# Optimization experiments

Hardware: AMD Instinct MI355X
Metric: run time of the kernel (lower is better)

Reference implementation:

```python
import jax, jax.numpy as jnp
import numpy as np

DIM = 1024
HEADS = 16
HEAD_DIM = DIM // HEADS
MLP_HID = 4 * DIM
EPS = 1e-5


def layer_norm(x, g, b):
    mu = jnp.mean(x, axis=-1, keepdims=True)
    var = jnp.mean(jnp.square(x - mu), axis=-1, keepdims=True)
    return (x - mu) * jax.lax.rsqrt(var + EPS) * g + b


def setup_inputs() -> dict:
    key = jax.random.key(0)
    ks = jax.random.split(key, 8)
    s_in = 1.0 / np.sqrt(DIM)
    s_hid = 1.0 / np.sqrt(MLP_HID)
    return {
        "x": jax.random.normal(ks[0], (4, 2048, DIM), dtype=jnp.float32),
        "qkv_w": jax.random.uniform(ks[1], (3 * DIM, DIM), jnp.float32, -s_in, s_in),
        "proj_w": jax.random.uniform(ks[2], (DIM, DIM), jnp.float32, -s_in, s_in),
        "proj_b": jnp.zeros((DIM,), jnp.float32),
        "ln1_g": jnp.ones((DIM,), jnp.float32),
        "ln1_b": jnp.zeros((DIM,), jnp.float32),
        "w1": jax.random.uniform(ks[3], (MLP_HID, DIM), jnp.float32, -s_in, s_in),
        "b1": jnp.zeros((MLP_HID,), jnp.float32),
        "prelu_a": jnp.asarray(0.25, jnp.float32),
        "w2": jax.random.uniform(ks[4], (DIM, MLP_HID), jnp.float32, -s_hid, s_hid),
        "b2": jnp.zeros((DIM,), jnp.float32),
        "ln2_g": jnp.ones((DIM,), jnp.float32),
        "ln2_b": jnp.zeros((DIM,), jnp.float32),
    }


def reference(x, qkv_w, proj_w, proj_b, ln1_g, ln1_b, w1, b1, prelu_a, w2, b2, ln2_g, ln2_b):
    B, N, C = x.shape
    scale = HEAD_DIM ** (-0.5)

    # Multi-head self-attention (full NxN scores, softmax over keys)
    qkv = (x @ qkv_w.T).reshape(B, N, 3, HEADS, HEAD_DIM)
    qkv = jnp.transpose(qkv, (2, 0, 3, 1, 4))  # [3, B, H, N, hd]
    q, k, v = qkv[0] * scale, qkv[1], qkv[2]
    attn = jax.nn.softmax(jnp.einsum("bhnd,bhmd->bhnm", q, k), axis=-1)
    o = jnp.einsum("bhnm,bhmd->bhnd", attn, v)
    o = jnp.transpose(o, (0, 2, 1, 3)).reshape(B, N, C)
    o = o @ proj_w.T + proj_b

    # Post-norm residual 1
    x = layer_norm(x + o, ln1_g, ln1_b)

    # MLP: Linear -> (Dropout=identity in eval) -> PReLU -> Linear
    h = x @ w1.T + b1
    h = jnp.where(h >= 0, h, prelu_a * h)
    h = h @ w2.T + b2

    # Post-norm residual 2
    return layer_norm(x + h, ln2_g, ln2_b)
```

## Files before the change

### kernel.cpp

```cpp
#include <hip/hip_runtime.h>


typedef __attribute__((ext_vector_type(8))) short short8;
typedef __attribute__((ext_vector_type(4))) short short4v;
typedef __attribute__((ext_vector_type(4))) float floatx4;
typedef __attribute__((ext_vector_type(4))) int int4v;

__device__ __forceinline__ float bf2f(unsigned short u) {
    return __uint_as_float(((unsigned int)u) << 16);
}
__device__ __forceinline__ unsigned short f2bf(float f) {
    unsigned int u = __float_as_uint(f);
    u += 0x7FFFu + ((u >> 16) & 1u);
    return (unsigned short)(u >> 16);
}
__device__ __forceinline__ int pack2bf(float a, float b) {
    return (int)f2bf(a) | ((int)f2bf(b) << 16);
}
__device__ __forceinline__ unsigned int cvt_pk_bf16(float lo, float hi) {
    unsigned int r;
    asm("v_cvt_pk_bf16_f32 %0, %1, %2" : "=v"(r) : "v"(lo), "v"(hi));
    return r;
}

#define Q_PRESCALE 0.18033688011112043f

#if __has_builtin(__builtin_amdgcn_exp2f)
__device__ __forceinline__ float fast_exp2(float x) { return __builtin_amdgcn_exp2f(x); }
#else
__device__ __forceinline__ float fast_exp2(float x) { return __expf(x * 0.6931471805599453f); }
#endif

#if __has_builtin(__builtin_amdgcn_permlane32_swap) && __has_builtin(__builtin_amdgcn_permlane16_swap)
#define HAVE_PERMLANE 1
#else
#define HAVE_PERMLANE 0
#endif

__device__ __forceinline__ void async16(const unsigned short* g, unsigned short* l) {
    __builtin_amdgcn_global_load_lds(
        (const __attribute__((address_space(1))) unsigned int*)g,
        (__attribute__((address_space(3))) unsigned int*)l, 16, 0, 0);
}

#define BARRIER() do { __builtin_amdgcn_s_barrier(); asm volatile("" ::: "memory"); } while (0)
#define VMCNT(n)  asm volatile("s_waitcnt vmcnt(" #n ")" ::: "memory")
#define LGKM0()   asm volatile("s_waitcnt lgkmcnt(0)" ::: "memory")

__global__ __launch_bounds__(256)
void cvt_f2b(const float* __restrict__ in, unsigned short* __restrict__ out) {
    const int i = (blockIdx.x * 256 + threadIdx.x) * 4;
    float4 v = *(const float4*)&in[i];
    short4v o;
    o[0] = (short)f2bf(v.x); o[1] = (short)f2bf(v.y);
    o[2] = (short)f2bf(v.z); o[3] = (short)f2bf(v.w);
    *(short4v*)&out[i] = o;
}

__global__ __launch_bounds__(256)
void cvt_weights(const float* __restrict__ qkv_w, const float* __restrict__ proj_w,
                 const float* __restrict__ w1, const float* __restrict__ w2,
                 unsigned short* __restrict__ dst) {
    const int b = blockIdx.x;
    const float* src;
    int off;
    if (b < 3072)      { src = qkv_w;  off = b; }
    else if (b < 4096) { src = proj_w; off = b - 3072; }
    else if (b < 8192) { src = w1;     off = b - 4096; }
    else               { src = w2;     off = b - 8192; }
    const size_t si = (size_t)off * 1024 + threadIdx.x * 4;
    const size_t di = (size_t)b   * 1024 + threadIdx.x * 4;
    float4 v = *(const float4*)&src[si];
    short4v o;
    o[0] = (short)f2bf(v.x); o[1] = (short)f2bf(v.y);
    o[2] = (short)f2bf(v.z); o[3] = (short)f2bf(v.w);
    *(short4v*)&dst[di] = o;
}

__global__ __launch_bounds__(512, 2)
void gemm256(const unsigned short* __restrict__ A,
             const unsigned short* __restrict__ W,
             const float* __restrict__ bias,
             const float* __restrict__ prelu,
             unsigned short* __restrict__ C,
             int N, int K, int qcols, int NNT) {
    __shared__ alignas(16) unsigned short lA[2][256 * 64];
    __shared__ alignas(16) unsigned short lB[2][256 * 64];

    const int nwg = gridDim.x;
    const int orig = blockIdx.x;
    const int q8 = nwg >> 3, r8 = nwg & 7, xx = orig & 7, rest = orig >> 3;
    const int wgid = (xx < r8 ? xx * (q8 + 1) : r8 * (q8 + 1) + (xx - r8) * q8) + rest;
    const int mt = wgid / NNT, nt = wgid % NNT;
    const int m0 = mt * 256, n0 = nt * 256;

    const int tid  = threadIdx.x;
    const int lane = tid & 63;
    const int wave = tid >> 6;
    const int lr = lane & 15, lq = lane >> 4;
    const int wrow = (wave >> 2) * 64;
    const int wcol = (wave & 3) * 32;
    const int srow = lane >> 3;
    const int scol = ((lane & 7) ^ srow) << 3;
    const int kx = lr & 7;

    const int NT = K >> 6;

    floatx4 acc[2][2][4][2] = {};
    short8 af[4][2], b0[2][2], b1[2][2];

    auto stA = [&](int d, int tt, int h) {
        #pragma unroll
        for (int it = 0; it < 2; ++it) {
            const int rb = h * 128 + (wave * 2 + it) * 8;
            async16(&A[(size_t)(m0 + rb + srow) * K + tt * 64 + scol], &lA[d][rb * 64]);
        }
    };
    auto stB = [&](int d, int tt, int h) {
        #pragma unroll
        for (int it = 0; it < 2; ++it) {
            const int rb = h * 128 + (wave * 2 + it) * 8;
            async16(&W[(size_t)(n0 + rb + srow) * K + tt * 64 + scol], &lB[d][rb * 64]);
        }
    };

#define RD_AF(dd, half)                                                        \
    _Pragma("unroll") for (int i = 0; i < 4; ++i)                              \
    _Pragma("unroll") for (int s = 0; s < 2; ++s)                              \
        af[i][s] = *(const short8*)&lA[dd][((half) * 128 + wrow + i * 16 + lr) * 64 + \
                                           (((s * 4 + lq) ^ kx) << 3)]
#define RD_B0(dd)                                                              \
    _Pragma("unroll") for (int j = 0; j < 2; ++j)                              \
    _Pragma("unroll") for (int s = 0; s < 2; ++s)                              \
        b0[j][s] = *(const short8*)&lB[dd][(wcol + j * 16 + lr) * 64 +         \
                                           (((s * 4 + lq) ^ kx) << 3)]
#define RD_B1(dd)                                                              \
    _Pragma("unroll") for (int j = 0; j < 2; ++j)                              \
    _Pragma("unroll") for (int s = 0; s < 2; ++s)                              \
        b1[j][s] = *(const short8*)&lB[dd][(128 + wcol + j * 16 + lr) * 64 +   \
                                           (((s * 4 + lq) ^ kx) << 3)]
#define MM256(mh, nh, BB)                                                      \
    _Pragma("unroll") for (int s = 0; s < 2; ++s)                              \
    _Pragma("unroll") for (int i = 0; i < 4; ++i)                              \
    _Pragma("unroll") for (int j = 0; j < 2; ++j)                              \
        acc[mh][nh][i][j] = __builtin_amdgcn_mfma_f32_16x16x32_bf16(           \
            af[i][s], BB[j][s], acc[mh][nh][i][j], 0, 0, 0)

    stA(0, 0, 0); stB(0, 0, 0); stB(0, 0, 1); stA(0, 0, 1);
    stA(1, 1, 0); stB(1, 1, 0); stB(1, 1, 1);
    VMCNT(6);
    BARRIER();
    RD_AF(0, 0);
    RD_B0(0);

    auto tile = [&](int t, int d, int e) {
        RD_B1(d);
        if (t + 1 < NT) stA(e, t + 1, 1);
        BARRIER();
        __builtin_amdgcn_s_setprio(1);
        MM256(0, 0, b0);
        __builtin_amdgcn_s_setprio(0);
        BARRIER();

        if (t + 2 < NT) stA(d, t + 2, 0);
        BARRIER();
        __builtin_amdgcn_s_setprio(1);
        MM256(0, 1, b1);
        __builtin_amdgcn_s_setprio(0);
        RD_AF(d, 1);
        BARRIER();

        if (t + 2 < NT) stB(d, t + 2, 0);
        BARRIER();
        __builtin_amdgcn_s_setprio(1);
        MM256(1, 1, b1);
        __builtin_amdgcn_s_setprio(0);
        if (t + 2 < NT)      { VMCNT(4); }
        else if (t + 1 < NT) { VMCNT(0); }
        BARRIER();

        if (t + 2 < NT) stB(d, t + 2, 1);
        BARRIER();
        __builtin_amdgcn_s_setprio(1);
        MM256(1, 0, b0);
        __builtin_amdgcn_s_setprio(0);
        if (t + 1 < NT) {
            RD_AF(e, 0);
            RD_B0(e);
        }
        BARRIER();
    };

    for (int t = 0; t < NT; t += 2) {
        tile(t, 0, 1);
        tile(t + 1, 1, 0);
    }

#undef RD_AF
#undef RD_B0
#undef RD_B1
#undef MM256

    const bool hasb = (bias != nullptr);
    const bool hasp = (prelu != nullptr);
    const float slope = hasp ? prelu[0] : 0.f;
    #pragma unroll
    for (int mh = 0; mh < 2; ++mh)
        #pragma unroll
        for (int nh = 0; nh < 2; ++nh)
            #pragma unroll
            for (int j = 0; j < 2; ++j) {
                const int gc = n0 + nh * 128 + wcol + j * 16 + lr;
                const float bv = hasb ? bias[gc] : 0.f;
                const float cs = (gc < qcols) ? Q_PRESCALE : 1.f;
                #pragma unroll
                for (int i = 0; i < 4; ++i) {
                    const int gr = m0 + mh * 128 + wrow + i * 16 + lq * 4;
                    #pragma unroll
                    for (int r = 0; r < 4; ++r) {
                        float v = acc[mh][nh][i][j][r] + bv;
                        if (hasp && v < 0.f) v *= slope;
                        C[(size_t)(gr + r) * N + gc] = f2bf(v * cs);
                    }
                }
            }
}

__global__ __launch_bounds__(512, 2)
void gemm128(const unsigned short* __restrict__ A,
             const unsigned short* __restrict__ W,
             const float* __restrict__ bias,
             const float* __restrict__ prelu,
             unsigned short* __restrict__ C,
             int N, int K, int qcols, int NNT) {
    __shared__ alignas(16) unsigned short lA[2][128 * 64];
    __shared__ alignas(16) unsigned short lB[2][256 * 64];

    const int nwg = gridDim.x;
    const int orig = blockIdx.x;
    const int q8 = nwg >> 3, r8 = nwg & 7, xx = orig & 7, rest = orig >> 3;
    const int wgid = (xx < r8 ? xx * (q8 + 1) : r8 * (q8 + 1) + (xx - r8) * q8) + rest;
    const int mt = wgid / NNT, nt = wgid % NNT;
    const int m0 = mt * 128, n0 = nt * 256;

    const int tid  = threadIdx.x;
    const int lane = tid & 63;
    const int wave = tid >> 6;
    const int lr = lane & 15, lq = lane >> 4;
    const int wrow = (wave >> 2) * 64;
    const int wcol = (wave & 3) * 32;
    const int srow = lane >> 3;
    const int scol = ((lane & 7) ^ srow) << 3;
    const int kx = lr & 7;

    const int NT = K >> 6;

    floatx4 acc[2][4][2] = {};
    short8 af[4][2], b0[2][2], b1[2][2];

    auto stA = [&](int d, int tt) {
        #pragma unroll
        for (int it = 0; it < 2; ++it) {
            const int rb = (wave * 2 + it) * 8;
            async16(&A[(size_t)(m0 + rb + srow) * K + tt * 64 + scol], &lA[d][rb * 64]);
        }
    };
    auto stB = [&](int d, int tt, int h) {
        #pragma unroll
        for (int it = 0; it < 2; ++it) {
            const int rb = (wave * 2 + it) * 8;
            async16(&W[(size_t)(n0 + h * 128 + rb + srow) * K + tt * 64 + scol],
                    &lB[d][(h * 128 + rb) * 64]);
        }
    };

#define RD_AF(dd)                                                              \
    _Pragma("unroll") for (int i = 0; i < 4; ++i)                              \
    _Pragma("unroll") for (int s = 0; s < 2; ++s)                              \
        af[i][s] = *(const short8*)&lA[dd][(wrow + i * 16 + lr) * 64 +         \
                                           (((s * 4 + lq) ^ kx) << 3)]
#define RD_B0(dd)                                                              \
    _Pragma("unroll") for (int j = 0; j < 2; ++j)                              \
    _Pragma("unroll") for (int s = 0; s < 2; ++s)                              \
        b0[j][s] = *(const short8*)&lB[dd][(wcol + j * 16 + lr) * 64 +         \
                                           (((s * 4 + lq) ^ kx) << 3)]
#define RD_B1(dd)                                                              \
    _Pragma("unroll") for (int j = 0; j < 2; ++j)                              \
    _Pragma("unroll") for (int s = 0; s < 2; ++s)                              \
        b1[j][s] = *(const short8*)&lB[dd][(128 + wcol + j * 16 + lr) * 64 +   \
                                           (((s * 4 + lq) ^ kx) << 3)]
#define MM128(nh, BB)                                                          \
    _Pragma("unroll") for (int s = 0; s < 2; ++s)                              \
    _Pragma("unroll") for (int i = 0; i < 4; ++i)                              \
    _Pragma("unroll") for (int j = 0; j < 2; ++j)                              \
        acc[nh][i][j] = __builtin_amdgcn_mfma_f32_16x16x32_bf16(               \
            af[i][s], BB[j][s], acc[nh][i][j], 0, 0, 0)

    stA(0, 0); stB(0, 0, 0); stB(0, 0, 1);
    stA(1, 1); stB(1, 1, 0);
    VMCNT(4);
    BARRIER();

    auto tile = [&](int t, int d, int e) {
        RD_AF(d);
        RD_B0(d);
        if (t + 1 < NT) stB(e, t + 1, 1);
        BARRIER();
        LGKM0();
        __builtin_amdgcn_s_setprio(1);
        MM128(0, b0);
        __builtin_amdgcn_s_setprio(0);
        BARRIER();

        RD_B1(d);
        if (t + 2 < NT) { stA(d, t + 2); stB(d, t + 2, 0); }
        BARRIER();
        LGKM0();
        __builtin_amdgcn_s_setprio(1);
        MM128(1, b1);
        __builtin_amdgcn_s_setprio(0);
        if (t + 2 < NT)      { VMCNT(4); }
        else if (t + 1 < NT) { VMCNT(0); }
        BARRIER();
    };

    for (int t = 0; t < NT; t += 2) {
        tile(t, 0, 1);
        tile(t + 1, 1, 0);
    }

#undef RD_AF
#undef RD_B0
#undef RD_B1
#undef MM128

    const bool hasb = (bias != nullptr);
    const bool hasp = (prelu != nullptr);
    const float slope = hasp ? prelu[0] : 0.f;
    #pragma unroll
    for (int nh = 0; nh < 2; ++nh)
        #pragma unroll
        for (int j = 0; j < 2; ++j) {
            const int gc = n0 + nh * 128 + wcol + j * 16 + lr;
            const float bv = hasb ? bias[gc] : 0.f;
            const float cs = (gc < qcols) ? Q_PRESCALE : 1.f;
            #pragma unroll
            for (int i = 0; i < 4; ++i) {
                const int gr = m0 + wrow + i * 16 + lq * 4;
                #pragma unroll
                for (int r = 0; r < 4; ++r) {
                    float v = acc[nh][i][j][r] + bv;
                    if (hasp && v < 0.f) v *= slope;
                    C[(size_t)(gr + r) * N + gc] = f2bf(v * cs);
                }
            }
        }
}

__global__ __launch_bounds__(256)
void transpose_v(const unsigned short* __restrict__ qkv,
                 unsigned short* __restrict__ vt) {
    const int kt = blockIdx.x;
    const int bh = blockIdx.y;
    const int b = bh >> 4, h = bh & 15;
    __shared__ unsigned short tile[64 * 65];
    for (int t = threadIdx.x; t < 512; t += 256) {
        const int key = t >> 3, c8 = (t & 7) << 3;
        short8 v8 = *(const short8*)&qkv[((size_t)(b * 2048 + kt * 64 + key)) * 3072 +
                                         2048 + h * 64 + c8];
        #pragma unroll
        for (int e = 0; e < 8; ++e)
            tile[key * 65 + c8 + e] = (unsigned short)v8[e];
    }
    __syncthreads();
    for (int t = threadIdx.x; t < 512; t += 256) {
        const int d = t >> 3, k8 = (t & 7) << 3;
        short8 o;
        #pragma unroll
        for (int e = 0; e < 8; ++e)
            o[e] = (short)tile[(k8 + e) * 65 + d];
        *(short8*)&vt[((size_t)bh * 64 + d) * 2048 + kt * 64 + k8] = o;
    }
}

__global__ __launch_bounds__(256, 2)
void attn_kernel(const unsigned short* __restrict__ qkv,
                 const unsigned short* __restrict__ vt,
                 unsigned short* __restrict__ o_attn) {
    const int id = blockIdx.x;
    const int qg = id >> 6;
    const int bh = id & 63;
    const int b = bh >> 4, h = bh & 15;
    const int tid  = threadIdx.x;
    const int lane = tid & 63;
    const int wave = tid >> 6;
    const int lr = lane & 15;
    const int lq = lane >> 4;
    const int q0 = (qg * 4 + wave) * 64;
    const size_t row0 = (size_t)(b * 2048) * 3072;

    __shared__ alignas(16) unsigned short lK[2][64 * 64];
    __shared__ alignas(16) unsigned short lV[2][64 * 64];

    short8 qf[4][2];
    #pragma unroll
    for (int j = 0; j < 4; ++j)
        #pragma unroll
        for (int s = 0; s < 2; ++s)
            qf[j][s] = *(const short8*)&qkv[row0 + (size_t)(q0 + j * 16 + lr) * 3072 +
                                            h * 64 + s * 32 + lq * 8];

    floatx4 oacc[4][4] = {};
    float l_i[4] = {0.f, 0.f, 0.f, 0.f};

    const int srow = lane >> 3;
    const int scol = (((lane & 7) ^ srow)) << 3;
    const int kx = lr & 7;

    auto stage = [&](int bi, int kc) {
        #pragma unroll
        for (int it2 = 0; it2 < 2; ++it2) {
            const int it = wave * 2 + it2;
            const int row = it * 8 + srow;
            async16(&qkv[row0 + (size_t)(kc + row) * 3072 + 1024 + h * 64 + scol],
                    &lK[bi][it * 512 + lane * 8]);
            async16(&vt[((size_t)bh * 64 + row) * 2048 + kc + scol],
                    &lV[bi][it * 512 + lane * 8]);
        }
    };

    asm volatile("s_waitcnt vmcnt(0)" ::: "memory");
    stage(0, 0);

    #pragma unroll 1
    for (int c = 0; c < 32; ++c) {
        const int cur = c & 1;
        if (c + 1 < 32) {
            stage(cur ^ 1, (c + 1) * 64);
            asm volatile("s_waitcnt vmcnt(4)" ::: "memory");
        } else {
            asm volatile("s_waitcnt vmcnt(0)" ::: "memory");
        }
        __builtin_amdgcn_s_barrier();
        asm volatile("" ::: "memory");

        floatx4 sacc[4][4] = {};
        #pragma unroll
        for (int s = 0; s < 2; ++s) {
            short8 kf[4];
            #pragma unroll
            for (int i = 0; i < 4; ++i) {
                const int r = i * 16 + lr;
                kf[i] = *(const short8*)&lK[cur][r * 64 + (((s * 4 + lq) ^ kx) << 3)];
            }
            __builtin_amdgcn_s_setprio(1);
            #pragma unroll
            for (int i = 0; i < 4; ++i)
                #pragma unroll
                for (int j = 0; j < 4; ++j)
                    sacc[i][j] = __builtin_amdgcn_mfma_f32_16x16x32_bf16(
                        kf[i], qf[j][s], sacc[i][j], 0, 0, 0);
            __builtin_amdgcn_s_setprio(0);
        }

        unsigned int pkd[4][4][2];
        #pragma unroll
        for (int i = 0; i < 4; ++i)
            #pragma unroll
            for (int j = 0; j < 4; ++j) {
                const float e0 = fast_exp2(sacc[i][j][0]);
                const float e1 = fast_exp2(sacc[i][j][1]);
                const float e2 = fast_exp2(sacc[i][j][2]);
                const float e3 = fast_exp2(sacc[i][j][3]);
                l_i[j] += (e0 + e1) + (e2 + e3);
                pkd[i][j][0] = cvt_pk_bf16(e0, e1);
                pkd[i][j][1] = cvt_pk_bf16(e2, e3);
            }

        #pragma unroll
        for (int s = 0; s < 2; ++s) {
            short8 vf[4];
            #pragma unroll
            for (int i = 0; i < 4; ++i) {
                const int r = i * 16 + lr;
                vf[i] = *(const short8*)&lV[cur][r * 64 + (((s * 4 + lq) ^ kx) << 3)];
            }
            short8 bq[4];
            #pragma unroll
            for (int j = 0; j < 4; ++j) {
                int4v iv;
#if HAVE_PERMLANE
                auto p0 = __builtin_amdgcn_permlane32_swap(
                    pkd[2 * s][j][0], pkd[2 * s + 1][j][0], false, false);
                auto w0 = __builtin_amdgcn_permlane16_swap(p0[0], p0[1], false, false);
                auto p1 = __builtin_amdgcn_permlane32_swap(
                    pkd[2 * s][j][1], pkd[2 * s + 1][j][1], false, false);
                auto w1 = __builtin_amdgcn_permlane16_swap(p1[0], p1[1], false, false);
                iv[0] = (int)w0[0]; iv[1] = (int)w1[0];
                iv[2] = (int)w0[1]; iv[3] = (int)w1[1];
#else
                const int src0 = lr + ((lq & 1) * 2) * 16;
                const int src1 = src0 + 16;
                const bool hi = (lq >> 1) != 0;
                int a0 = __shfl((int)pkd[2 * s][j][0], src0, 64);
                int c0 = __shfl((int)pkd[2 * s + 1][j][0], src0, 64);
                int a1 = __shfl((int)pkd[2 * s][j][1], src0, 64);
                int c1 = __shfl((int)pkd[2 * s + 1][j][1], src0, 64);
                int a2 = __shfl((int)pkd[2 * s][j][0], src1, 64);
                int c2 = __shfl((int)pkd[2 * s + 1][j][0], src1, 64);
                int a3 = __shfl((int)pkd[2 * s][j][1], src1, 64);
                int c3 = __shfl((int)pkd[2 * s + 1][j][1], src1, 64);
                iv[0] = hi ? c0 : a0;
                iv[1] = hi ? c1 : a1;
                iv[2] = hi ? c2 : a2;
                iv[3] = hi ? c3 : a3;
#endif
                bq[j] = __builtin_bit_cast(short8, iv);
            }
            __builtin_amdgcn_s_setprio(1);
            #pragma unroll
            for (int j = 0; j < 4; ++j)
                #pragma unroll
                for (int i = 0; i < 4; ++i)
                    oacc[i][j] = __builtin_amdgcn_mfma_f32_16x16x32_bf16(
                        vf[i], bq[j], oacc[i][j], 0, 0, 0);
            __builtin_amdgcn_s_setprio(0);
        }

        asm volatile("s_waitcnt lgkmcnt(0)" ::: "memory");
        __builtin_amdgcn_s_barrier();
        asm volatile("" ::: "memory");
    }

    #pragma unroll
    for (int j = 0; j < 4; ++j) {
        l_i[j] += __shfl_xor(l_i[j], 16, 64);
        l_i[j] += __shfl_xor(l_i[j], 32, 64);
        const float rl = 1.f / l_i[j];
        const int q = q0 + j * 16 + lr;
        #pragma unroll
        for (int i = 0; i < 4; ++i) {
            int2 pk;
            pk.x = pack2bf(oacc[i][j][0] * rl, oacc[i][j][1] * rl);
            pk.y = pack2bf(oacc[i][j][2] * rl, oacc[i][j][3] * rl);
            *(int2*)&o_attn[((size_t)(b * 2048 + q)) * 1024 + h * 64 + i * 16 + lq * 4] = pk;
        }
    }
}

__global__ __launch_bounds__(256)
void ln_f32_bf16(const float* __restrict__ x,
                 const unsigned short* __restrict__ res,
                 const float* __restrict__ g,
                 const float* __restrict__ bta,
                 unsigned short* __restrict__ out) {
    const int row = blockIdx.x;
    const int t = threadIdx.x;
    const size_t base = (size_t)row * 1024;

    float4 xv = *(const float4*)&x[base + t * 4];
    short4v rv = *(const short4v*)&res[base + t * 4];
    float v[4] = { xv.x + bf2f((unsigned short)rv[0]),
                   xv.y + bf2f((unsigned short)rv[1]),
                   xv.z + bf2f((unsigned short)rv[2]),
                   xv.w + bf2f((unsigned short)rv[3]) };
    float s = 0.f, s2 = 0.f;
    #pragma unroll
    for (int k = 0; k < 4; ++k) { s += v[k]; s2 += v[k] * v[k]; }
    #pragma unroll
    for (int off = 32; off > 0; off >>= 1) {
        s  += __shfl_xor(s, off, 64);
        s2 += __shfl_xor(s2, off, 64);
    }
    __shared__ float red[8];
    const int wave = t >> 6;
    if ((t & 63) == 0) { red[wave] = s; red[4 + wave] = s2; }
    __syncthreads();
    s  = red[0] + red[1] + red[2] + red[3];
    s2 = red[4] + red[5] + red[6] + red[7];
    const float mean = s * (1.f / 1024.f);
    const float var  = fmaxf(s2 * (1.f / 1024.f) - mean * mean, 0.f);
    const float inv  = rsqrtf(var + 1e-5f);

    short4v ov;
    #pragma unroll
    for (int k = 0; k < 4; ++k) {
        int c = t * 4 + k;
        ov[k] = (short)f2bf((v[k] - mean) * inv * g[c] + bta[c]);
    }
    *(short4v*)&out[base + t * 4] = ov;
}

__global__ __launch_bounds__(256)
void ln_bf16_f32(const unsigned short* __restrict__ x,
                 const unsigned short* __restrict__ res,
                 const float* __restrict__ g,
                 const float* __restrict__ bta,
                 float* __restrict__ out) {
    const int row = blockIdx.x;
    const int t = threadIdx.x;
    const size_t base = (size_t)row * 1024;

    short4v xv = *(const short4v*)&x[base + t * 4];
    short4v rv = *(const short4v*)&res[base + t * 4];
    float v[4];
    float s = 0.f, s2 = 0.f;
    #pragma unroll
    for (int k = 0; k < 4; ++k) {
        v[k] = bf2f((unsigned short)xv[k]) + bf2f((unsigned short)rv[k]);
        s += v[k];
        s2 += v[k] * v[k];
    }
    #pragma unroll
    for (int off = 32; off > 0; off >>= 1) {
        s  += __shfl_xor(s, off, 64);
        s2 += __shfl_xor(s2, off, 64);
    }
    __shared__ float red[8];
    const int wave = t >> 6;
    if ((t & 63) == 0) { red[wave] = s; red[4 + wave] = s2; }
    __syncthreads();
    s  = red[0] + red[1] + red[2] + red[3];
    s2 = red[4] + red[5] + red[6] + red[7];
    const float mean = s * (1.f / 1024.f);
    const float var  = fmaxf(s2 * (1.f / 1024.f) - mean * mean, 0.f);
    const float inv  = rsqrtf(var + 1e-5f);

    float4 ov;
    ov.x = (v[0] - mean) * inv * g[t * 4 + 0] + bta[t * 4 + 0];
    ov.y = (v[1] - mean) * inv * g[t * 4 + 1] + bta[t * 4 + 1];
    ov.z = (v[2] - mean) * inv * g[t * 4 + 2] + bta[t * 4 + 2];
    ov.w = (v[3] - mean) * inv * g[t * 4 + 3] + bta[t * 4 + 3];
    *(float4*)&out[base + t * 4] = ov;
}

extern "C" void kernel_launch(void* const* d_in, const int* in_sizes, int n_in,
                              void* d_out, int out_size, void* d_ws, size_t ws_size,
                              hipStream_t stream) {
    const float* x      = (const float*)d_in[0];
    const float* qkv_w  = (const float*)d_in[1];
    const float* proj_w = (const float*)d_in[2];
    const float* proj_b = (const float*)d_in[3];
    const float* ln1_g  = (const float*)d_in[4];
    const float* ln1_b  = (const float*)d_in[5];
    const float* w1     = (const float*)d_in[6];
    const float* b1     = (const float*)d_in[7];
    const float* prelu  = (const float*)d_in[8];
    const float* w2     = (const float*)d_in[9];
    const float* b2     = (const float*)d_in[10];
    const float* ln2_g  = (const float*)d_in[11];
    const float* ln2_b  = (const float*)d_in[12];
    float* out = (float*)d_out;

    char* ws = (char*)d_ws;
    const size_t MB = 1024 * 1024;
    unsigned short* wqkvb  = (unsigned short*)(ws);
    unsigned short* wprojb = (unsigned short*)(ws + 6 * MB);
    unsigned short* w1b    = (unsigned short*)(ws + 8 * MB);
    unsigned short* w2b    = (unsigned short*)(ws + 16 * MB);
    unsigned short* xb     = (unsigned short*)(ws + 24 * MB);
    unsigned short* vtb    = (unsigned short*)(ws + 24 * MB);
    unsigned short* qkvb   = (unsigned short*)(ws + 40 * MB);
    unsigned short* oat    = (unsigned short*)(ws + 88 * MB);
    unsigned short* pout   = (unsigned short*)(ws + 24 * MB);
    unsigned short* x1b    = (unsigned short*)(ws + 40 * MB);
    unsigned short* h1     = (unsigned short*)(ws + 56 * MB);
    unsigned short* h2     = (unsigned short*)(ws + 24 * MB);

    cvt_f2b<<<8192, 256, 0, stream>>>(x, xb);
    cvt_weights<<<12288, 256, 0, stream>>>(qkv_w, proj_w, w1, w2,
                                           (unsigned short*)ws);

    gemm128<<<dim3(64 * 12), 512, 0, stream>>>(xb, wqkvb, nullptr, nullptr,
                                               qkvb, 3072, 1024, 1024, 12);
    transpose_v<<<dim3(32, 64), 256, 0, stream>>>(qkvb, vtb);
    attn_kernel<<<512, 256, 0, stream>>>(qkvb, vtb, oat);
    gemm128<<<dim3(64 * 4), 512, 0, stream>>>(oat, wprojb, proj_b, nullptr,
                                              pout, 1024, 1024, 0, 4);
    ln_f32_bf16<<<8192, 256, 0, stream>>>(x, pout, ln1_g, ln1_b, x1b);
    gemm256<<<dim3(32 * 16), 512, 0, stream>>>(x1b, w1b, b1, prelu,
                                               h1, 4096, 1024, 0, 16);
    gemm128<<<dim3(64 * 4), 512, 0, stream>>>(h1, w2b, b2, nullptr,
                                              h2, 1024, 4096, 0, 4);
    ln_bf16_f32<<<8192, 256, 0, stream>>>(x1b, h2, ln2_g, ln2_b, out);
}
```

Measured before the change: 488.7 us.

## Add 128x128 GEMM for N=1024 projections, drop 256x256 GEMM, fuse conversions

Adds a 4-wave 128x128-tile GEMM (gemm_sq) with a simpler double-buffered pipeline and uses it for the proj and w2 GEMMs, doubling their workgroup count to 512 to fill more CUs. The w1 GEMM switches from the 256x256 kernel to the 128x256 kernel, also with more workgroups. The two fp32-to-bf16 conversion kernels are merged into one launch. The trade is more parallelism against less data reuse per tile and a gemm_sq loop that waits on all outstanding loads (vmcnt(0)) every tile.

Result: no change. 493.3 us (+0.9%).

```diff
diff --git a/kernel.cpp b/kernel.cpp
--- a/kernel.cpp
+++ b/kernel.cpp
@@ -48,43 +48,40 @@
 #define LGKM0()   asm volatile("s_waitcnt lgkmcnt(0)" ::: "memory")
 
 __global__ __launch_bounds__(256)
-void cvt_f2b(const float* __restrict__ in, unsigned short* __restrict__ out) {
-    const int i = (blockIdx.x * 256 + threadIdx.x) * 4;
-    float4 v = *(const float4*)&in[i];
+void cvt_all(const float* __restrict__ x, const float* __restrict__ qkv_w,
+             const float* __restrict__ proj_w, const float* __restrict__ w1,
+             const float* __restrict__ w2,
+             unsigned short* __restrict__ xb, unsigned short* __restrict__ wb) {
+    const int b = blockIdx.x;
+    const float* src;
+    unsigned short* dst;
+    size_t doff;
+    if (b < 8192) {
+        src = x + (size_t)b * 1024; dst = xb; doff = (size_t)b * 1024;
+    } else {
+        const int wk = b - 8192;
+        dst = wb; doff = (size_t)wk * 1024;
+        if (wk < 3072)      src = qkv_w  + (size_t)wk * 1024;
+        else if (wk < 4096) src = proj_w + (size_t)(wk - 3072) * 1024;
+        else if (wk < 8192) src = w1     + (size_t)(wk - 4096) * 1024;
+        else                src = w2     + (size_t)(wk - 8192) * 1024;
+    }
+    const int t4 = threadIdx.x * 4;
+    float4 v = *(const float4*)&src[t4];
     short4v o;
     o[0] = (short)f2bf(v.x); o[1] = (short)f2bf(v.y);
     o[2] = (short)f2bf(v.z); o[3] = (short)f2bf(v.w);
-    *(short4v*)&out[i] = o;
-}
-
-__global__ __launch_bounds__(256)
-void cvt_weights(const float* __restrict__ qkv_w, const float* __restrict__ proj_w,
-                 const float* __restrict__ w1, const float* __restrict__ w2,
-                 unsigned short* __restrict__ dst) {
-    const int b = blockIdx.x;
-    const float* src;
-    int off;
-    if (b < 3072)      { src = qkv_w;  off = b; }
-    else if (b < 4096) { src = proj_w; off = b - 3072; }
-    else if (b < 8192) { src = w1;     off = b - 4096; }
-    else               { src = w2;     off = b - 8192; }
-    const size_t si = (size_t)off * 1024 + threadIdx.x * 4;
-    const size_t di = (size_t)b   * 1024 + threadIdx.x * 4;
-    float4 v = *(const float4*)&src[si];
-    short4v o;
-    o[0] = (short)f2bf(v.x); o[1] = (short)f2bf(v.y);
-    o[2] = (short)f2bf(v.z); o[3] = (short)f2bf(v.w);
-    *(short4v*)&dst[di] = o;
+    *(short4v*)&dst[doff + t4] = o;
 }
 
 __global__ __launch_bounds__(512, 2)
-void gemm256(const unsigned short* __restrict__ A,
+void gemm128(const unsigned short* __restrict__ A,
              const unsigned short* __restrict__ W,
              const float* __restrict__ bias,
              const float* __restrict__ prelu,
              unsigned short* __restrict__ C,
              int N, int K, int qcols, int NNT) {
-    __shared__ alignas(16) unsigned short lA[2][256 * 64];
+    __shared__ alignas(16) unsigned short lA[2][128 * 64];
     __shared__ alignas(16) unsigned short lB[2][256 * 64];
 
     const int nwg = gridDim.x;
@@ -92,7 +89,7 @@
     const int q8 = nwg >> 3, r8 = nwg & 7, xx = orig & 7, rest = orig >> 3;
     const int wgid = (xx < r8 ? xx * (q8 + 1) : r8 * (q8 + 1) + (xx - r8) * q8) + rest;
     const int mt = wgid / NNT, nt = wgid % NNT;
-    const int m0 = mt * 256, n0 = nt * 256;
+    const int m0 = mt * 128, n0 = nt * 256;
 
     const int tid  = threadIdx.x;
     const int lane = tid & 63;
@@ -106,155 +103,6 @@
 
     const int NT = K >> 6;
 
-    floatx4 acc[2][2][4][2] = {};
-    short8 af[4][2], b0[2][2], b1[2][2];
-
-    auto stA = [&](int d, int tt, int h) {
-        #pragma unroll
-        for (int it = 0; it < 2; ++it) {
-            const int rb = h * 128 + (wave * 2 + it) * 8;
-            async16(&A[(size_t)(m0 + rb + srow) * K + tt * 64 + scol], &lA[d][rb * 64]);
-        }
-    };
-    auto stB = [&](int d, int tt, int h) {
-        #pragma unroll
-        for (int it = 0; it < 2; ++it) {
-            const int rb = h * 128 + (wave * 2 + it) * 8;
-            async16(&W[(size_t)(n0 + rb + srow) * K + tt * 64 + scol], &lB[d][rb * 64]);
-        }
-    };
-
-#define RD_AF(dd, half)                                                        \
-    _Pragma("unroll") for (int i = 0; i < 4; ++i)                              \
-    _Pragma("unroll") for (int s = 0; s < 2; ++s)                              \
-        af[i][s] = *(const short8*)&lA[dd][((half) * 128 + wrow + i * 16 + lr) * 64 + \
-                                           (((s * 4 + lq) ^ kx) << 3)]
-#define RD_B0(dd)                                                              \
-    _Pragma("unroll") for (int j = 0; j < 2; ++j)                              \
-    _Pragma("unroll") for (int s = 0; s < 2; ++s)                              \
-        b0[j][s] = *(const short8*)&lB[dd][(wcol + j * 16 + lr) * 64 +         \
-                                           (((s * 4 + lq) ^ kx) << 3)]
-#define RD_B1(dd)                                                              \
-    _Pragma("unroll") for (int j = 0; j < 2; ++j)                              \
-    _Pragma("unroll") for (int s = 0; s < 2; ++s)                              \
-        b1[j][s] = *(const short8*)&lB[dd][(128 + wcol + j * 16 + lr) * 64 +   \
-                                           (((s * 4 + lq) ^ kx) << 3)]
-#define MM256(mh, nh, BB)                                                      \
-    _Pragma("unroll") for (int s = 0; s < 2; ++s)                              \
-    _Pragma("unroll") for (int i = 0; i < 4; ++i)                              \
-    _Pragma("unroll") for (int j = 0; j < 2; ++j)                              \
-        acc[mh][nh][i][j] = __builtin_amdgcn_mfma_f32_16x16x32_bf16(           \
-            af[i][s], BB[j][s], acc[mh][nh][i][j], 0, 0, 0)
-
-    stA(0, 0, 0); stB(0, 0, 0); stB(0, 0, 1); stA(0, 0, 1);
-    stA(1, 1, 0); stB(1, 1, 0); stB(1, 1, 1);
-    VMCNT(6);
-    BARRIER();
-    RD_AF(0, 0);
-    RD_B0(0);
-
-    auto tile = [&](int t, int d, int e) {
-        RD_B1(d);
-        if (t + 1 < NT) stA(e, t + 1, 1);
-        BARRIER();
-        __builtin_amdgcn_s_setprio(1);
-        MM256(0, 0, b0);
-        __builtin_amdgcn_s_setprio(0);
-        BARRIER();
-
-        if (t + 2 < NT) stA(d, t + 2, 0);
-        BARRIER();
-        __builtin_amdgcn_s_setprio(1);
-        MM256(0, 1, b1);
-        __builtin_amdgcn_s_setprio(0);
-        RD_AF(d, 1);
-        BARRIER();
-
-        if (t + 2 < NT) stB(d, t + 2, 0);
-        BARRIER();
-        __builtin_amdgcn_s_setprio(1);
-        MM256(1, 1, b1);
-        __builtin_amdgcn_s_setprio(0);
-        if (t + 2 < NT)      { VMCNT(4); }
-        else if (t + 1 < NT) { VMCNT(0); }
-        BARRIER();
-
-        if (t + 2 < NT) stB(d, t + 2, 1);
-        BARRIER();
-        __builtin_amdgcn_s_setprio(1);
-        MM256(1, 0, b0);
-        __builtin_amdgcn_s_setprio(0);
-        if (t + 1 < NT) {
-            RD_AF(e, 0);
-            RD_B0(e);
-        }
-        BARRIER();
-    };
-
-    for (int t = 0; t < NT; t += 2) {
-        tile(t, 0, 1);
-        tile(t + 1, 1, 0);
-    }
-
-#undef RD_AF
-#undef RD_B0
-#undef RD_B1
-#undef MM256
-
-    const bool hasb = (bias != nullptr);
-    const bool hasp = (prelu != nullptr);
-    const float slope = hasp ? prelu[0] : 0.f;
-    #pragma unroll
-    for (int mh = 0; mh < 2; ++mh)
-        #pragma unroll
-        for (int nh = 0; nh < 2; ++nh)
-            #pragma unroll
-            for (int j = 0; j < 2; ++j) {
-                const int gc = n0 + nh * 128 + wcol + j * 16 + lr;
-                const float bv = hasb ? bias[gc] : 0.f;
-                const float cs = (gc < qcols) ? Q_PRESCALE : 1.f;
-                #pragma unroll
-                for (int i = 0; i < 4; ++i) {
-                    const int gr = m0 + mh * 128 + wrow + i * 16 + lq * 4;
-                    #pragma unroll
-                    for (int r = 0; r < 4; ++r) {
-                        float v = acc[mh][nh][i][j][r] + bv;
-                        if (hasp && v < 0.f) v *= slope;
-                        C[(size_t)(gr + r) * N + gc] = f2bf(v * cs);
-                    }
-                }
-            }
-}
-
-__global__ __launch_bounds__(512, 2)
-void gemm128(const unsigned short* __restrict__ A,
-             const unsigned short* __restrict__ W,
-             const float* __restrict__ bias,
-             const float* __restrict__ prelu,
-             unsigned short* __restrict__ C,
-             int N, int K, int qcols, int NNT) {
-    __shared__ alignas(16) unsigned short lA[2][128 * 64];
-    __shared__ alignas(16) unsigned short lB[2][256 * 64];
-
-    const int nwg = gridDim.x;
-    const int orig = blockIdx.x;
-    const int q8 = nwg >> 3, r8 = nwg & 7, xx = orig & 7, rest = orig >> 3;
-    const int wgid = (xx < r8 ? xx * (q8 + 1) : r8 * (q8 + 1) + (xx - r8) * q8) + rest;
-    const int mt = wgid / NNT, nt = wgid % NNT;
-    const int m0 = mt * 128, n0 = nt * 256;
-
-    const int tid  = threadIdx.x;
-    const int lane = tid & 63;
-    const int wave = tid >> 6;
-    const int lr = lane & 15, lq = lane >> 4;
-    const int wrow = (wave >> 2) * 64;
-    const int wcol = (wave & 3) * 32;
-    const int srow = lane >> 3;
-    const int scol = ((lane & 7) ^ srow) << 3;
-    const int kx = lr & 7;
-
-    const int NT = K >> 6;
-
     floatx4 acc[2][4][2] = {};
     short8 af[4][2], b0[2][2], b1[2][2];
 
@@ -355,6 +203,132 @@
                 }
             }
         }
+}
+
+__global__ __launch_bounds__(256, 2)
+void gemm_sq(const unsigned short* __restrict__ A,
+             const unsigned short* __restrict__ W,
+             const float* __restrict__ bias,
+             const float* __restrict__ prelu,
+             unsigned short* __restrict__ C,
+             int N, int K, int qcols, int NNT) {
+    __shared__ alignas(16) unsigned short lA[2][128 * 64];
+    __shared__ alignas(16) unsigned short lB[2][128 * 64];
+
+    const int nwg = gridDim.x;
+    const int orig = blockIdx.x;
+    const int q8 = nwg >> 3, r8 = nwg & 7, xx = orig & 7, rest = orig >> 3;
+    const int wgid = (xx < r8 ? xx * (q8 + 1) : r8 * (q8 + 1) + (xx - r8) * q8) + rest;
+    const int mt = wgid / NNT, nt = wgid % NNT;
+    const int m0 = mt * 128, n0 = nt * 128;
+
+    const int tid  = threadIdx.x;
+    const int lane = tid & 63;
+    const int wave = tid >> 6;
+    const int lr = lane & 15, lq = lane >> 4;
+    const int wrow = (wave >> 1) * 64;
+    const int wcol = (wave & 1) * 64;
+    const int srow = lane >> 3;
+    const int scol = ((lane & 7) ^ srow) << 3;
+    const int kx = lr & 7;
+
+    const int NT = K >> 6;
+
+    floatx4 acc[4][4] = {};
+    short8 af[4][2], b0[2][2], b1[2][2];
+
+    auto stA = [&](int d, int tt) {
+        #pragma unroll
+        for (int it = 0; it < 4; ++it) {
+            const int rb = it * 32 + wave * 8;
+            async16(&A[(size_t)(m0 + rb + srow) * K + tt * 64 + scol], &lA[d][rb * 64]);
+        }
+    };
+    auto stB = [&](int d, int tt) {
+        #pragma unroll
+        for (int it = 0; it < 4; ++it) {
+            const int rb = it * 32 + wave * 8;
+            async16(&W[(size_t)(n0 + rb + srow) * K + tt * 64 + scol], &lB[d][rb * 64]);
+        }
+    };
+
+#define RD_AF(dd)                                                              \
+    _Pragma("unroll") for (int i = 0; i < 4; ++i)                              \
+    _Pragma("unroll") for (int s = 0; s < 2; ++s)                              \
+        af[i][s] = *(const short8*)&lA[dd][(wrow + i * 16 + lr) * 64 +         \
+                                           (((s * 4 + lq) ^ kx) << 3)]
+#define RD_B0(dd)                                                              \
+    _Pragma("unroll") for (int j = 0; j < 2; ++j)                              \
+    _Pragma("unroll") for (int s = 0; s < 2; ++s)                              \
+        b0[j][s] = *(const short8*)&lB[dd][(wcol + j * 16 + lr) * 64 +         \
+                                           (((s * 4 + lq) ^ kx) << 3)]
+#define RD_B1(dd)                                                              \
+    _Pragma("unroll") for (int j = 0; j < 2; ++j)                              \
+    _Pragma("unroll") for (int s = 0; s < 2; ++s)                              \
+        b1[j][s] = *(const short8*)&lB[dd][(wcol + 32 + j * 16 + lr) * 64 +    \
+                                           (((s * 4 + lq) ^ kx) << 3)]
+#define MMSQ(jb, BB)                                                           \
+    _Pragma("unroll") for (int s = 0; s < 2; ++s)                              \
+    _Pragma("unroll") for (int i = 0; i < 4; ++i)                              \
+    _Pragma("unroll") for (int j = 0; j < 2; ++j)                              \
+        acc[i][(jb) + j] = __builtin_amdgcn_mfma_f32_16x16x32_bf16(            \
+            af[i][s], BB[j][s], acc[i][(jb) + j], 0, 0, 0)
+
+    stA(0, 0); stB(0, 0);
+    VMCNT(0);
+    BARRIER();
+
+    auto tile = [&](int t, int d, int e) {
+        RD_AF(d);
+        RD_B0(d);
+        if (t + 1 < NT) stA(e, t + 1);
+        BARRIER();
+        LGKM0();
+        __builtin_amdgcn_s_setprio(1);
+        MMSQ(0, b0);
+        __builtin_amdgcn_s_setprio(0);
+        BARRIER();
+
+        RD_B1(d);
+        if (t + 1 < NT) stB(e, t + 1);
+        BARRIER();
+        LGKM0();
+        __builtin_amdgcn_s_setprio(1);
+        MMSQ(2, b1);
+        __builtin_amdgcn_s_setprio(0);
+        VMCNT(0);
+        BARRIER();
+    };
+
+    for (int t = 0; t < NT; t += 2) {
+        tile(t, 0, 1);
+        tile(t + 1, 1, 0);
+    }
+
+#undef RD_AF
+#undef RD_B0
+#undef RD_B1
+#undef MMSQ
+
+    const bool hasb = (bias != nullptr);
+    const bool hasp = (prelu != nullptr);
+    const float slope = hasp ? prelu[0] : 0.f;
+    #pragma unroll
+    for (int j = 0; j < 4; ++j) {
+        const int gc = n0 + wcol + j * 16 + lr;
+        const float bv = hasb ? bias[gc] : 0.f;
+        const float cs = (gc < qcols) ? Q_PRESCALE : 1.f;
+        #pragma unroll
+        for (int i = 0; i < 4; ++i) {
+            const int gr = m0 + wrow + i * 16 + lq * 4;
+            #pragma unroll
+            for (int r = 0; r < 4; ++r) {
+                float v = acc[i][j][r] + bv;
+                if (hasp && v < 0.f) v *= slope;
+                C[(size_t)(gr + r) * N + gc] = f2bf(v * cs);
+            }
+        }
+    }
 }
 
 __global__ __launch_bounds__(256)
@@ -667,20 +641,19 @@
     unsigned short* h1     = (unsigned short*)(ws + 56 * MB);
     unsigned short* h2     = (unsigned short*)(ws + 24 * MB);
 
-    cvt_f2b<<<8192, 256, 0, stream>>>(x, xb);
-    cvt_weights<<<12288, 256, 0, stream>>>(qkv_w, proj_w, w1, w2,
-                                           (unsigned short*)ws);
+    cvt_all<<<20480, 256, 0, stream>>>(x, qkv_w, proj_w, w1, w2,
+                                       xb, (unsigned short*)ws);
 
     gemm128<<<dim3(64 * 12), 512, 0, stream>>>(xb, wqkvb, nullptr, nullptr,
                                                qkvb, 3072, 1024, 1024, 12);
     transpose_v<<<dim3(32, 64), 256, 0, stream>>>(qkvb, vtb);
     attn_kernel<<<512, 256, 0, stream>>>(qkvb, vtb, oat);
-    gemm128<<<dim3(64 * 4), 512, 0, stream>>>(oat, wprojb, proj_b, nullptr,
-                                              pout, 1024, 1024, 0, 4);
+    gemm_sq<<<dim3(64 * 8), 256, 0, stream>>>(oat, wprojb, proj_b, nullptr,
+                                              pout, 1024, 1024, 0, 8);
     ln_f32_bf16<<<8192, 256, 0, stream>>>(x, pout, ln1_g, ln1_b, x1b);
-    gemm256<<<dim3(32 * 16), 512, 0, stream>>>(x1b, w1b, b1, prelu,
+    gemm128<<<dim3(64 * 16), 512, 0, stream>>>(x1b, w1b, b1, prelu,
                                                h1, 4096, 1024, 0, 16);
-    gemm128<<<dim3(64 * 4), 512, 0, stream>>>(h1, w2b, b2, nullptr,
-                                              h2, 1024, 4096, 0, 4);
+    gemm_sq<<<dim3(64 * 8), 256, 0, stream>>>(h1, w2b, b2, nullptr,
+                                              h2, 1024, 4096, 0, 8);
     ln_bf16_f32<<<8192, 256, 0, stream>>>(x1b, h2, ln2_g, ln2_b, out);
 }
```
